# Kernel optimization log

Hardware: AMD Instinct MI355X
Metric: run time of the kernel (lower is better)

Reference implementation:

```python
import jax, jax.numpy as jnp
import numpy as np

EMBED_DIM = 768
HIDDEN_DIM = 384          # max(embed_dim // 2, 128)
NUM_HEADS = 12
HEAD_DIM = EMBED_DIM // NUM_HEADS
LAYER_VOCAB = 4           # len(target_layers)
THRESHOLD = 0.5
MIN_KEEP_RATIO = 0.1
B, N = 8, 1024


def setup_inputs() -> dict:
    key = jax.random.key(0)
    ks = jax.random.split(key, 12)
    std = 0.02
    return {
        "tokens": jax.random.normal(ks[0], (B, N, EMBED_DIM), jnp.float32),
        "layer_token_idx": 1,
        # actor params
        "layer_emb": jax.random.normal(ks[1], (LAYER_VOCAB, EMBED_DIM), jnp.float32) * std,
        "ln_g": jnp.ones((EMBED_DIM,), jnp.float32),
        "ln_b": jnp.zeros((EMBED_DIM,), jnp.float32),
        "w1": jax.random.normal(ks[2], (HIDDEN_DIM, EMBED_DIM), jnp.float32) * std,
        "b1": jnp.zeros((HIDDEN_DIM,), jnp.float32),
        "w2": jax.random.normal(ks[3], (HIDDEN_DIM, HIDDEN_DIM), jnp.float32) * std,
        "b2": jnp.zeros((HIDDEN_DIM,), jnp.float32),
        "w3": jax.random.normal(ks[4], (1, HIDDEN_DIM), jnp.float32) * std,
        "b3": jnp.zeros((1,), jnp.float32),
        # attention params (timm-style)
        "qkv_w": jax.random.normal(ks[5], (3 * EMBED_DIM, EMBED_DIM), jnp.float32) * std,
        "qkv_b": jnp.zeros((3 * EMBED_DIM,), jnp.float32),
        "proj_w": jax.random.normal(ks[6], (EMBED_DIM, EMBED_DIM), jnp.float32) * std,
        "proj_b": jnp.zeros((EMBED_DIM,), jnp.float32),
    }


def _layernorm(x, g, b, eps=1e-5):
    mu = x.mean(-1, keepdims=True)
    var = ((x - mu) ** 2).mean(-1, keepdims=True)
    return (x - mu) * jax.lax.rsqrt(var + eps) * g + b


def _forward(tokens, layer_token_idx, layer_emb, ln_g, ln_b, w1, b1, w2, b2, w3, b3,
             qkv_w, qkv_b, proj_w, proj_b):
    Bsz, Ntok, C = tokens.shape
    # --- MAPPOActor: logits ---
    ctx = tokens + layer_emb[layer_token_idx]               # broadcast [C]
    ctx = ctx + ctx.mean(axis=1, keepdims=True)             # global context
    h = _layernorm(ctx, ln_g, ln_b)
    h = jax.nn.gelu(h @ w1.T + b1, approximate=False)
    h = jax.nn.gelu(h @ w2.T + b2, approximate=False)
    logits = (h @ w3.T + b3).squeeze(-1)                    # [B, N]
    probs = jax.nn.sigmoid(logits)
    # --- compute_mask: threshold + min-keep topk correction ---
    binary = probs >= THRESHOLD                             # [B, N] bool
    min_keep = max(int(Ntok * MIN_KEEP_RATIO), 1)
    min_keep = min(min_keep, Ntok)
    _, topk_idx = jax.lax.top_k(probs, min_keep)            # [B, min_keep]
    fixed = jnp.zeros((Bsz, Ntok), bool).at[jnp.arange(Bsz)[:, None], topk_idx].set(True)
    need_fix = binary.sum(-1) < min_keep                    # [B]
    mask = jnp.where(need_fix[:, None], fixed, binary)
    mask = mask.at[:, 0].set(True)
    # --- masked attention (timm style) ---
    qkv = tokens @ qkv_w.T + qkv_b                          # [B, N, 3C]
    qkv = qkv.reshape(Bsz, Ntok, 3, NUM_HEADS, HEAD_DIM).transpose(2, 0, 3, 1, 4)
    q, k, v = qkv[0], qkv[1], qkv[2]                        # [B, H, N, D]
    q = q * (HEAD_DIM ** -0.5)
    scores = jnp.einsum("bhnd,bhmd->bhnm", q, k)            # [B, H, N, N]
    neg = jnp.finfo(scores.dtype).min
    scores = jnp.where(mask[:, None, None, :], scores, neg)
    attn = jax.nn.softmax(scores, axis=-1)
    v = v * mask[:, None, :, None].astype(v.dtype)
    out = jnp.einsum("bhnm,bhmd->bhnd", attn, v)
    out = out.transpose(0, 2, 1, 3).reshape(Bsz, Ntok, C)
    out = out @ proj_w.T + proj_b
    out = out * mask[..., None].astype(out.dtype)           # zero_out_queries=True
    return out


def reference(tokens, layer_token_idx, layer_emb, ln_g, ln_b, w1, b1, w2, b2, w3, b3,
              qkv_w, qkv_b, proj_w, proj_b):
    return _forward(tokens, layer_token_idx, layer_emb, ln_g, ln_b, w1, b1, w2, b2,
                    w3, b3, qkv_w, qkv_b, proj_w, proj_b)
```

## Files before the change

### kernel.cpp

```cpp
#include <hip/hip_runtime.h>
#include <cstdint>
#include <cmath>

#define EMBED 768
#define HID 384
#define NHEAD 12
#define HDIM 64
#define BATCH 8
#define NTOK 1024
#define MINKEEP 102

using f32x4  = __attribute__((ext_vector_type(4))) float;
using short8 = __attribute__((ext_vector_type(8))) short;
using short4v = __attribute__((ext_vector_type(4))) short;
using half8  = __attribute__((ext_vector_type(8))) _Float16;

__device__ inline short f2bf(float f) {
  unsigned u = __float_as_uint(f);
  u += 0x7fffu + ((u >> 16) & 1u);
  return (short)(u >> 16);
}
__device__ inline float bf2f(short s) {
  return __uint_as_float(((unsigned)(unsigned short)s) << 16);
}
__device__ inline unsigned pack_bf2(float lo, float hi) {
  unsigned ul = __float_as_uint(lo);
  ul += 0x7fffu + ((ul >> 16) & 1u);
  unsigned uh = __float_as_uint(hi);
  uh += 0x7fffu + ((uh >> 16) & 1u);
  return (ul >> 16) | (uh & 0xffff0000u);
}
__device__ inline void split2h(float v, short& h, short& m) {
  _Float16 h0 = (_Float16)v;
  float r = v - (float)h0;
  _Float16 m0 = (_Float16)r;
  h = __builtin_bit_cast(short, h0);
  m = __builtin_bit_cast(short, m0);
}

__global__ __launch_bounds__(256) void prep_kernel(
    const float* __restrict__ qkv_w, short* __restrict__ wq_bf,
    const float* __restrict__ proj_w, short* __restrict__ wp_bf,
    const float* __restrict__ w1, short* __restrict__ w1h, short* __restrict__ w1m,
    const float* __restrict__ w2, short* __restrict__ w2h, short* __restrict__ w2m,
    const float* __restrict__ layer_emb, const int* __restrict__ lidx,
    float* __restrict__ addvec) {
  int blk = blockIdx.x, tid = threadIdx.x;
  if (blk < 2304) {
    const float* in = (blk < 1728) ? qkv_w : proj_w;
    short* out = (blk < 1728) ? wq_bf : wp_bf;
    int i = (blk < 1728 ? blk : blk - 1728) * 256 + tid;
    float4 f = ((const float4*)in)[i];
    short4v s;
    s[0] = f2bf(f.x); s[1] = f2bf(f.y); s[2] = f2bf(f.z); s[3] = f2bf(f.w);
    ((short4v*)out)[i] = s;
  } else if (blk < 2736) {
    const float* in = (blk < 2592) ? w1 : w2;
    short* oh = (blk < 2592) ? w1h : w2h;
    short* om = (blk < 2592) ? w1m : w2m;
    int i = (blk < 2592 ? blk - 2304 : blk - 2592) * 256 + tid;
    float4 f = ((const float4*)in)[i];
    short4v h, m;
    short th, tm;
    split2h(f.x, th, tm); h[0] = th; m[0] = tm;
    split2h(f.y, th, tm); h[1] = th; m[1] = tm;
    split2h(f.z, th, tm); h[2] = th; m[2] = tm;
    split2h(f.w, th, tm); h[3] = th; m[3] = tm;
    ((short4v*)oh)[i] = h;
    ((short4v*)om)[i] = m;
  } else {
    int i = (blk - 2736) * 256 + tid;
    int c = i & (EMBED - 1);
    c = i % EMBED;
    addvec[i] = 2.0f * layer_emb[lidx[0] * EMBED + c];
  }
}

__global__ __launch_bounds__(768) void colmean_kernel(
    const float* __restrict__ tokens, float* __restrict__ addvec) {
  int b = blockIdx.x, chunk = blockIdx.y, c = threadIdx.x;
  const float* tb = tokens + ((size_t)b * NTOK + chunk * 64) * EMBED + c;
  float s = 0.f;
#pragma unroll 8
  for (int n = 0; n < 64; ++n) s += tb[(size_t)n * EMBED];
  atomicAdd(&addvec[b * EMBED + c], s * (1.0f / NTOK));
}

__global__ __launch_bounds__(256) void ln_split_kernel(
    const float* __restrict__ tokens, const float* __restrict__ addvec,
    const float* __restrict__ gamma, const float* __restrict__ beta,
    short* __restrict__ xh, short* __restrict__ xm,
    short* __restrict__ tok_bf) {
  int row = blockIdx.x;
  int b = row >> 10;
  __shared__ float s_row[EMBED];
  __shared__ float s_red[4];
  const float* tr = tokens + (size_t)row * EMBED;
  const float* av = addvec + b * EMBED;
  float lsum = 0.f;
  for (int c = threadIdx.x; c < EMBED; c += 256) {
    float t = tr[c];
    tok_bf[(size_t)row * EMBED + c] = f2bf(t);
    float v = t + av[c];
    s_row[c] = v;
    lsum += v;
  }
  for (int o = 32; o; o >>= 1) lsum += __shfl_down(lsum, o, 64);
  int wid = threadIdx.x >> 6;
  if ((threadIdx.x & 63) == 0) s_red[wid] = lsum;
  __syncthreads();
  float mu = (s_red[0] + s_red[1] + s_red[2] + s_red[3]) * (1.f / EMBED);
  float lss = 0.f;
  for (int c = threadIdx.x; c < EMBED; c += 256) {
    float d = s_row[c] - mu;
    lss += d * d;
  }
  for (int o = 32; o; o >>= 1) lss += __shfl_down(lss, o, 64);
  __syncthreads();
  if ((threadIdx.x & 63) == 0) s_red[wid] = lss;
  __syncthreads();
  float var = (s_red[0] + s_red[1] + s_red[2] + s_red[3]) * (1.f / EMBED);
  float rinv = 1.0f / sqrtf(var + 1e-5f);
  for (int c = threadIdx.x; c < EMBED; c += 256) {
    float v = (s_row[c] - mu) * rinv * gamma[c] + beta[c];
    short h, m;
    split2h(v, h, m);
    size_t idx = (size_t)row * EMBED + c;
    xh[idx] = h; xm[idx] = m;
  }
}

__device__ inline float gelu_exact(float x) {
  return 0.5f * x * (1.0f + erff(x * 0.70710678118654752f));
}

template <int OUT>
__global__ __launch_bounds__(256) void gemm_split_kernel(
    const short* __restrict__ Ah, const short* __restrict__ Am,
    const short* __restrict__ Wh, const short* __restrict__ Wm,
    const float* __restrict__ bias, short* __restrict__ Ch,
    short* __restrict__ Cm, const float* __restrict__ w3,
    float* __restrict__ lgt, int M, int N, int K) {
  __shared__ short sA[2][64][40];
  __shared__ short sW[2][64][40];
  int tid = threadIdx.x;
  int w = tid >> 6, l = tid & 63, lg = l >> 4, lb = l & 15;
  int wr = (w >> 1) * 32, wc = (w & 1) * 32;
  int row0 = blockIdx.x * 64, col0 = blockIdx.y * 64;
  int srow = tid >> 2;
  int skk = (tid & 3) * 8;
  f32x4 acc0[2][2] = {}, acc1[2][2] = {};
  short8 ra0, ra1, rw0, rw1;
  {
    size_t aoff = (size_t)(row0 + srow) * K + skk;
    size_t woff = (size_t)(col0 + srow) * K + skk;
    ra0 = *(const short8*)(Ah + aoff);
    ra1 = *(const short8*)(Am + aoff);
    rw0 = *(const short8*)(Wh + woff);
    rw1 = *(const short8*)(Wm + woff);
  }
  for (int k0 = 0; k0 < K; k0 += 32) {
    __syncthreads();
    *(short8*)&sA[0][srow][skk] = ra0;
    *(short8*)&sA[1][srow][skk] = ra1;
    *(short8*)&sW[0][srow][skk] = rw0;
    *(short8*)&sW[1][srow][skk] = rw1;
    __syncthreads();
    if (k0 + 32 < K) {
      size_t aoff = (size_t)(row0 + srow) * K + k0 + 32 + skk;
      size_t woff = (size_t)(col0 + srow) * K + k0 + 32 + skk;
      ra0 = *(const short8*)(Ah + aoff);
      ra1 = *(const short8*)(Am + aoff);
      rw0 = *(const short8*)(Wh + woff);
      rw1 = *(const short8*)(Wm + woff);
    }
    half8 ah[2], am[2], bh[2], bm[2];
#pragma unroll
    for (int i = 0; i < 2; ++i) {
      ah[i] = *(half8*)&sA[0][wr + i * 16 + lb][lg * 8];
      am[i] = *(half8*)&sA[1][wr + i * 16 + lb][lg * 8];
      bh[i] = *(half8*)&sW[0][wc + i * 16 + lb][lg * 8];
      bm[i] = *(half8*)&sW[1][wc + i * 16 + lb][lg * 8];
    }
#pragma unroll
    for (int i = 0; i < 2; ++i)
#pragma unroll
      for (int j = 0; j < 2; ++j) {
        f32x4 c0 = acc0[i][j];
        f32x4 c1 = acc1[i][j];
        c0 = __builtin_amdgcn_mfma_f32_16x16x32_f16(ah[i], bh[j], c0, 0, 0, 0);
        c1 = __builtin_amdgcn_mfma_f32_16x16x32_f16(ah[i], bm[j], c1, 0, 0, 0);
        c0 = __builtin_amdgcn_mfma_f32_16x16x32_f16(am[i], bh[j], c0, 0, 0, 0);
        acc0[i][j] = c0;
        acc1[i][j] = c1;
      }
  }
  if (OUT == 0) {
#pragma unroll
    for (int i = 0; i < 2; ++i) {
#pragma unroll
      for (int j = 0; j < 2; ++j) {
#pragma unroll
        for (int r = 0; r < 4; ++r) {
          int grow = row0 + wr + i * 16 + lg * 4 + r;
          int gcol = col0 + wc + j * 16 + lb;
          float g = gelu_exact(acc0[i][j][r] + acc1[i][j][r] + bias[gcol]);
          size_t idx = (size_t)grow * N + gcol;
          short h, m;
          split2h(g, h, m);
          Ch[idx] = h; Cm[idx] = m;
        }
      }
    }
  } else {
    float part[2][4];
#pragma unroll
    for (int i = 0; i < 2; ++i)
#pragma unroll
      for (int r = 0; r < 4; ++r) part[i][r] = 0.f;
#pragma unroll
    for (int i = 0; i < 2; ++i) {
#pragma unroll
      for (int j = 0; j < 2; ++j) {
#pragma unroll
        for (int r = 0; r < 4; ++r) {
          int gcol = col0 + wc + j * 16 + lb;
          float g = gelu_exact(acc0[i][j][r] + acc1[i][j][r] + bias[gcol]);
          part[i][r] += g * w3[gcol];
        }
      }
    }
#pragma unroll
    for (int i = 0; i < 2; ++i) {
#pragma unroll
      for (int r = 0; r < 4; ++r) {
        float v = part[i][r];
        v += __shfl_xor(v, 1);
        v += __shfl_xor(v, 2);
        v += __shfl_xor(v, 4);
        v += __shfl_xor(v, 8);
        if (lb == 0) atomicAdd(&lgt[row0 + wr + i * 16 + lg * 4 + r], v);
      }
    }
  }
}

__global__ __launch_bounds__(1024) void mask_kernel(
    const float* __restrict__ lgt, const float* __restrict__ b3,
    int* __restrict__ kidx, int* __restrict__ kc, float* __restrict__ biasc) {
  int b = blockIdx.x, tid = threadIdx.x;
  __shared__ unsigned long long keys[1024];
  __shared__ int flag[1024];
  __shared__ int wsum[16];
  float v = lgt[b * NTOK + tid] + b3[0];
  bool bin = (v >= 0.0f);
  int wid = tid >> 6, lane = tid & 63;
  unsigned long long bal = __ballot(bin);
  if (lane == 0) wsum[wid] = __popcll(bal);
  __syncthreads();
  int total = 0;
  for (int q = 0; q < 16; ++q) total += wsum[q];
  int mv;
  if (total >= MINKEEP) {
    mv = bin ? 1 : 0;
  } else {
    flag[tid] = 0;
    unsigned u = __float_as_uint(v);
    u = (u & 0x80000000u) ? ~u : (u | 0x80000000u);
    keys[tid] = ((unsigned long long)u << 32) | (unsigned)(1023 - tid);
    __syncthreads();
    for (int k2 = 2; k2 <= 1024; k2 <<= 1) {
      for (int j = k2 >> 1; j > 0; j >>= 1) {
        int ixj = tid ^ j;
        if (ixj > tid) {
          unsigned long long a = keys[tid], c = keys[ixj];
          bool desc = ((tid & k2) == 0);
          if (desc ? (a < c) : (a > c)) {
            keys[tid] = c;
            keys[ixj] = a;
          }
        }
        __syncthreads();
      }
    }
    if (tid < MINKEEP) {
      int idx = 1023 - (int)(keys[tid] & 0xFFFFFFFFu);
      flag[idx] = 1;
    }
    __syncthreads();
    mv = flag[tid];
  }
  if (tid == 0) mv = 1;
  __syncthreads();
  unsigned long long fb = __ballot(mv != 0);
  if (lane == 0) wsum[wid] = __popcll(fb);
  __syncthreads();
  int base = 0, tot = 0;
  for (int q = 0; q < 16; ++q) {
    int vq = wsum[q];
    if (q < wid) base += vq;
    tot += vq;
  }
  int pre = base + __popcll(fb & ((1ull << lane) - 1ull));
  if (mv) {
    kidx[b * NTOK + pre] = tid;
    biasc[b * NTOK + pre] = 0.f;
  }
  if (tid >= tot) {
    kidx[b * NTOK + tid] = 0;
    biasc[b * NTOK + tid] = -3.0e38f;
  }
  if (tid == 0) kc[b] = tot;
}

__global__ __launch_bounds__(256) void qkv_gather_kernel(
    const short* __restrict__ tok_bf, const short* __restrict__ W,
    const float* __restrict__ bias, const int* __restrict__ kidx,
    const int* __restrict__ kc, short* __restrict__ qq,
    short* __restrict__ kk_, short* __restrict__ vv) {
  __shared__ short sA[128][72];
  __shared__ short sW[128][72];
  __shared__ int s_idx[128];
  int bx = blockIdx.x;
  int b = bx & 7, bt = bx >> 3;
  int kcb = kc[b];
  if (bt * 128 >= kcb) return;
  int tid = threadIdx.x;
  if (tid < 128) s_idx[tid] = kidx[b * NTOK + bt * 128 + tid];
  int w = tid >> 6, l = tid & 63, lg = l >> 4, lb = l & 15;
  int wr = (w >> 1) * 64, wc = (w & 1) * 64;
  int col0 = blockIdx.y * 128;
  int r_ = tid >> 3, kq = (tid & 7) * 8;
  __syncthreads();
  const short* Ab = tok_bf + (size_t)b * NTOK * EMBED;
  f32x4 acc[4][4] = {};
  short8 pa[4], pw[4];
#pragma unroll
  for (int t = 0; t < 4; ++t) {
    pa[t] = *(const short8*)(Ab + (size_t)s_idx[t * 32 + r_] * EMBED + kq);
    pw[t] = *(const short8*)(W + (size_t)(col0 + t * 32 + r_) * EMBED + kq);
  }
  for (int k0 = 0; k0 < EMBED; k0 += 64) {
    __syncthreads();
#pragma unroll
    for (int t = 0; t < 4; ++t) {
      *(short8*)&sA[t * 32 + r_][kq] = pa[t];
      *(short8*)&sW[t * 32 + r_][kq] = pw[t];
    }
    __syncthreads();
    if (k0 + 64 < EMBED) {
#pragma unroll
      for (int t = 0; t < 4; ++t) {
        pa[t] = *(const short8*)(Ab + (size_t)s_idx[t * 32 + r_] * EMBED +
                                 k0 + 64 + kq);
        pw[t] = *(const short8*)(W + (size_t)(col0 + t * 32 + r_) * EMBED +
                                 k0 + 64 + kq);
      }
    }
#pragma unroll
    for (int half = 0; half < 2; ++half) {
      short8 af[4], bfr[4];
#pragma unroll
      for (int i = 0; i < 4; ++i)
        af[i] = *(short8*)&sA[wr + i * 16 + lb][half * 32 + lg * 8];
#pragma unroll
      for (int j = 0; j < 4; ++j)
        bfr[j] = *(short8*)&sW[wc + j * 16 + lb][half * 32 + lg * 8];
#pragma unroll
      for (int i = 0; i < 4; ++i)
#pragma unroll
        for (int j = 0; j < 4; ++j)
          acc[i][j] = __builtin_amdgcn_mfma_f32_16x16x32_bf16(af[i], bfr[j],
                                                              acc[i][j], 0, 0, 0);
    }
  }
#pragma unroll
  for (int i = 0; i < 4; ++i) {
#pragma unroll
    for (int j = 0; j < 4; ++j) {
#pragma unroll
      for (int r = 0; r < 4; ++r) {
        int jrow = bt * 128 + wr + i * 16 + lg * 4 + r;
        int gcol = col0 + wc + j * 16 + lb;
        float val = acc[i][j][r] + bias[gcol];
        int which = gcol / EMBED;
        int rem = gcol - which * EMBED;
        int h = rem >> 6, d = rem & 63;
        size_t dst = ((size_t)(b * NHEAD + h) * NTOK + jrow) * HDIM + d;
        if (which == 0)
          qq[dst] = f2bf(val * 0.125f);
        else if (which == 1)
          kk_[dst] = f2bf(val);
        else
          vv[dst] = f2bf(val);
      }
    }
  }
}

__global__ __launch_bounds__(256) void vtrans_kernel(
    const short* __restrict__ Vb, short* __restrict__ VT) {
  int bh = blockIdx.y;
  int n0 = blockIdx.x * 64;
  __shared__ short st[64][72];
  int tid = threadIdx.x;
#pragma unroll
  for (int t = 0; t < 2; ++t) {
    int c = tid + t * 256;
    int n = c >> 3, ds = c & 7;
    *(short8*)&st[n][ds * 8] =
        *(const short8*)(Vb + ((size_t)bh * NTOK + n0 + n) * HDIM + ds * 8);
  }
  __syncthreads();
#pragma unroll
  for (int t = 0; t < 2; ++t) {
    int c = tid + t * 256;
    int d = c >> 3, ns = c & 7;
    short8 tmp;
#pragma unroll
    for (int jj = 0; jj < 8; ++jj) tmp[jj] = st[ns * 8 + jj][d];
    *(short8*)(VT + ((size_t)bh * HDIM + d) * NTOK + n0 + ns * 8) = tmp;
  }
}

#define ATTN_SWZ(row, colbyte) (((row)*128) + ((colbyte) ^ (((row)&7) << 4)))

__global__ __launch_bounds__(256) void attn_mfma3_kernel(
    const short* __restrict__ Qc, const short* __restrict__ Kc,
    const short* __restrict__ VTc, const float* __restrict__ biasc,
    const int* __restrict__ kc, short* __restrict__ ao) {
  __shared__ __align__(16) short sK[64 * 64];
  __shared__ __align__(16) short sVT[64 * 64];
  int bid = blockIdx.x;
  int xcd = bid & 7, slot = bid >> 3;
  int bh = xcd * 12 + (slot >> 3);
  int qt = slot & 7;
  int b = bh / NHEAD;
  int kcb = kc[b];
  if (qt * 128 >= kcb) return;
  int nt = (kcb + 63) >> 6;
  int tid = threadIdx.x;
  int w = tid >> 6, l = tid & 63, lg = l >> 4, lb = l & 15;
  int n0 = qt * 128 + w * 32;
  const short* Qp = Qc + ((size_t)bh * NTOK + n0) * HDIM;
  const short* Kp = Kc + (size_t)bh * NTOK * HDIM;
  const short* Vp = VTc + (size_t)bh * HDIM * NTOK;
  const float* bp = biasc + b * NTOK;

  short8 qf[2][2];
#pragma unroll
  for (int i = 0; i < 2; ++i)
#pragma unroll
    for (int hh = 0; hh < 2; ++hh)
      qf[i][hh] = *(const short8*)(Qp + (i * 16 + lb) * HDIM + hh * 32 + lg * 8);

  f32x4 acc[2][4] = {};
  float lr[2] = {0.f, 0.f};

  int srow = tid >> 3;
  int scol = (tid & 7) * 8;
  int scolb = scol * 2;
  short8 rk0, rk1, rv0, rv1;

#define ATTN_LOADT(m0_)                                                        \
  {                                                                            \
    rk0 = *(const short8*)(Kp + (size_t)((m0_) + srow) * HDIM + scol);         \
    rk1 = *(const short8*)(Kp + (size_t)((m0_) + srow + 32) * HDIM + scol);    \
    rv0 = *(const short8*)(Vp + (size_t)srow * NTOK + (m0_) + scol);           \
    rv1 = *(const short8*)(Vp + (size_t)(srow + 32) * NTOK + (m0_) + scol);    \
  }

  ATTN_LOADT(0);
  for (int t = 0; t < nt; ++t) {
    int m0 = t * 64;
    *(short8*)((char*)sK + ATTN_SWZ(srow, scolb)) = rk0;
    *(short8*)((char*)sK + ATTN_SWZ(srow + 32, scolb)) = rk1;
    *(short8*)((char*)sVT + ATTN_SWZ(srow, scolb)) = rv0;
    *(short8*)((char*)sVT + ATTN_SWZ(srow + 32, scolb)) = rv1;
    __syncthreads();
    if (t + 1 < nt) ATTN_LOADT(m0 + 64);

    f32x4 bias4[4];
#pragma unroll
    for (int s = 0; s < 4; ++s)
      bias4[s] = *(const f32x4*)(bp + m0 + s * 16 + lg * 4);

    f32x4 S[2][4];
#pragma unroll
    for (int s = 0; s < 4; ++s) {
      short8 kf0 = *(const short8*)((const char*)sK +
                                    ATTN_SWZ(s * 16 + lb, lg * 16));
      short8 kf1 = *(const short8*)((const char*)sK +
                                    ATTN_SWZ(s * 16 + lb, 64 + lg * 16));
#pragma unroll
      for (int i = 0; i < 2; ++i) {
        f32x4 c = bias4[s];
        c = __builtin_amdgcn_mfma_f32_16x16x32_bf16(kf0, qf[i][0], c, 0, 0, 0);
        c = __builtin_amdgcn_mfma_f32_16x16x32_bf16(kf1, qf[i][1], c, 0, 0, 0);
        S[i][s] = c;
      }
    }

    unsigned pk[2][4][2];
#pragma unroll
    for (int i = 0; i < 2; ++i) {
      float rs = 0.f;
#pragma unroll
      for (int s = 0; s < 4; ++s) {
        float p0 = __expf(S[i][s][0]);
        float p1 = __expf(S[i][s][1]);
        float p2 = __expf(S[i][s][2]);
        float p3 = __expf(S[i][s][3]);
        rs += (p0 + p1) + (p2 + p3);
        pk[i][s][0] = pack_bf2(p0, p1);
        pk[i][s][1] = pack_bf2(p2, p3);
      }
      rs += __shfl_xor(rs, 16);
      rs += __shfl_xor(rs, 32);
      lr[i] += rs;
    }

    bool hi = (lg & 2) != 0;
    int srcl = ((lg & 1) * 2) * 16 + lb;
#pragma unroll
    for (int t2 = 0; t2 < 2; ++t2) {
      short8 vf[4];
#pragma unroll
      for (int u = 0; u < 4; ++u)
        vf[u] = *(const short8*)((const char*)sVT +
                                 ATTN_SWZ(u * 16 + lb, t2 * 64 + lg * 16));
#pragma unroll
      for (int i = 0; i < 2; ++i) {
        int a0 = __shfl((int)pk[i][2 * t2][0], srcl);
        int b0 = __shfl((int)pk[i][2 * t2 + 1][0], srcl);
        int a1 = __shfl((int)pk[i][2 * t2][1], srcl);
        int b1 = __shfl((int)pk[i][2 * t2 + 1][1], srcl);
        int a2 = __shfl((int)pk[i][2 * t2][0], srcl + 16);
        int b2 = __shfl((int)pk[i][2 * t2 + 1][0], srcl + 16);
        int a3 = __shfl((int)pk[i][2 * t2][1], srcl + 16);
        int b3 = __shfl((int)pk[i][2 * t2 + 1][1], srcl + 16);
        union { short8 s8; int u[4]; } pa;
        pa.u[0] = hi ? b0 : a0;
        pa.u[1] = hi ? b1 : a1;
        pa.u[2] = hi ? b2 : a2;
        pa.u[3] = hi ? b3 : a3;
#pragma unroll
        for (int u = 0; u < 4; ++u)
          acc[i][u] = __builtin_amdgcn_mfma_f32_16x16x32_bf16(pa.s8, vf[u],
                                                              acc[i][u], 0, 0, 0);
      }
    }
    __syncthreads();
  }

  int h = bh - b * NHEAD;
#pragma unroll
  for (int i = 0; i < 2; ++i) {
#pragma unroll
    for (int r = 0; r < 4; ++r) {
      float inv = 1.0f / __shfl(lr[i], lg * 4 + r);
      int j = n0 + i * 16 + lg * 4 + r;
#pragma unroll
      for (int u = 0; u < 4; ++u) {
        ao[((size_t)b * NTOK + j) * EMBED + h * HDIM + u * 16 + lb] =
            f2bf(acc[i][u][r] * inv);
      }
    }
  }
}

__global__ __launch_bounds__(256) void proj_gather_kernel(
    const short* __restrict__ A, const short* __restrict__ W,
    const float* __restrict__ bias, const int* __restrict__ kidx,
    const int* __restrict__ kc, float* __restrict__ out) {
  __shared__ short sA[128][72];
  __shared__ short sW[128][72];
  __shared__ int s_idx[128];
  int bx = blockIdx.x;
  int b = bx & 7, bt = bx >> 3;
  int kcb = kc[b];
  if (bt * 128 >= kcb) return;
  int tid = threadIdx.x;
  if (tid < 128) s_idx[tid] = kidx[b * NTOK + bt * 128 + tid];
  int w = tid >> 6, l = tid & 63, lg = l >> 4, lb = l & 15;
  int wr = (w >> 1) * 64, wc = (w & 1) * 64;
  int col0 = blockIdx.y * 128;
  int r_ = tid >> 3, kq = (tid & 7) * 8;
  const short* Ab = A + ((size_t)b * NTOK + bt * 128) * EMBED;
  f32x4 acc[4][4] = {};
  short8 pa[4], pw[4];
#pragma unroll
  for (int t = 0; t < 4; ++t) {
    pa[t] = *(const short8*)(Ab + (size_t)(t * 32 + r_) * EMBED + kq);
    pw[t] = *(const short8*)(W + (size_t)(col0 + t * 32 + r_) * EMBED + kq);
  }
  for (int k0 = 0; k0 < EMBED; k0 += 64) {
    __syncthreads();
#pragma unroll
    for (int t = 0; t < 4; ++t) {
      *(short8*)&sA[t * 32 + r_][kq] = pa[t];
      *(short8*)&sW[t * 32 + r_][kq] = pw[t];
    }
    __syncthreads();
    if (k0 + 64 < EMBED) {
#pragma unroll
      for (int t = 0; t < 4; ++t) {
        pa[t] = *(const short8*)(Ab + (size_t)(t * 32 + r_) * EMBED + k0 + 64 + kq);
        pw[t] = *(const short8*)(W + (size_t)(col0 + t * 32 + r_) * EMBED + k0 + 64 + kq);
      }
    }
#pragma unroll
    for (int half = 0; half < 2; ++half) {
      short8 af[4], bfr[4];
#pragma unroll
      for (int i = 0; i < 4; ++i)
        af[i] = *(short8*)&sA[wr + i * 16 + lb][half * 32 + lg * 8];
#pragma unroll
      for (int j = 0; j < 4; ++j)
        bfr[j] = *(short8*)&sW[wc + j * 16 + lb][half * 32 + lg * 8];
#pragma unroll
      for (int i = 0; i < 4; ++i)
#pragma unroll
        for (int j = 0; j < 4; ++j)
          acc[i][j] = __builtin_amdgcn_mfma_f32_16x16x32_bf16(af[i], bfr[j],
                                                              acc[i][j], 0, 0, 0);
    }
  }
#pragma unroll
  for (int i = 0; i < 4; ++i) {
#pragma unroll
    for (int j = 0; j < 4; ++j) {
#pragma unroll
      for (int r = 0; r < 4; ++r) {
        int jloc = wr + i * 16 + lg * 4 + r;
        int jrow = bt * 128 + jloc;
        int gcol = col0 + wc + j * 16 + lb;
        if (jrow < kcb) {
          int n = s_idx[jloc];
          out[((size_t)b * NTOK + n) * EMBED + gcol] = acc[i][j][r] + bias[gcol];
        }
      }
    }
  }
}

extern "C" void kernel_launch(void* const* d_in, const int* in_sizes, int n_in,
                              void* d_out, int out_size, void* d_ws, size_t ws_size,
                              hipStream_t stream) {
  const float* tokens   = (const float*)d_in[0];
  const int*   lidx     = (const int*)d_in[1];
  const float* layer_emb= (const float*)d_in[2];
  const float* ln_g     = (const float*)d_in[3];
  const float* ln_b     = (const float*)d_in[4];
  const float* w1       = (const float*)d_in[5];
  const float* b1       = (const float*)d_in[6];
  const float* w2       = (const float*)d_in[7];
  const float* b2       = (const float*)d_in[8];
  const float* w3       = (const float*)d_in[9];
  const float* b3       = (const float*)d_in[10];
  const float* qkv_w    = (const float*)d_in[11];
  const float* qkv_b    = (const float*)d_in[12];
  const float* proj_w   = (const float*)d_in[13];
  const float* proj_b   = (const float*)d_in[14];
  float* out = (float*)d_out;
  float* ws = (float*)d_ws;

  float* addvec = ws;
  float* lgt    = ws + 6144;
  int*   kidx   = (int*)(ws + 14336);
  float* biasc  = ws + 22528;
  int*   kc     = (int*)(ws + 30720);
  short* tok_bf = (short*)(ws + 30736);
  short* wq_bf  = (short*)(ws + 3176464);
  short* wp_bf  = (short*)(ws + 4061200);
  short* w1h = (short*)(ws + 4356112);
  short* w1m = (short*)(ws + 4503568);
  short* w2h = (short*)(ws + 4798480);
  short* w2m = (short*)(ws + 4872208);
  const size_t X0 = 5019664;
  short* xh  = (short*)(ws + X0);
  short* xm  = (short*)(ws + X0 + 3145728);
  short* h1h = (short*)(ws + X0 + 9437184);
  short* h1m = (short*)(ws + X0 + 11010048);
  short* Qc   = (short*)(ws + X0);
  short* Kc   = (short*)(ws + X0 + 3145728);
  short* Vc   = (short*)(ws + X0 + 6291456);
  short* VTc  = (short*)(ws + X0 + 9437184);
  short* aoc  = (short*)(ws + X0 + 12582912);

  hipMemsetAsync(d_out, 0, (size_t)out_size * sizeof(float), stream);
  hipMemsetAsync(lgt, 0, BATCH * NTOK * sizeof(float), stream);

  prep_kernel<<<dim3(2760), dim3(256), 0, stream>>>(
      qkv_w, wq_bf, proj_w, wp_bf, w1, w1h, w1m, w2, w2h, w2m,
      layer_emb, lidx, addvec);

  colmean_kernel<<<dim3(BATCH, 16), dim3(768), 0, stream>>>(tokens, addvec);
  ln_split_kernel<<<dim3(BATCH * NTOK), dim3(256), 0, stream>>>(
      tokens, addvec, ln_g, ln_b, xh, xm, tok_bf);
  gemm_split_kernel<0><<<dim3(128, 6), dim3(256), 0, stream>>>(
      xh, xm, w1h, w1m, b1, h1h, h1m, nullptr, nullptr,
      BATCH * NTOK, HID, EMBED);
  gemm_split_kernel<1><<<dim3(128, 6), dim3(256), 0, stream>>>(
      h1h, h1m, w2h, w2m, b2, nullptr, nullptr, w3, lgt,
      BATCH * NTOK, HID, HID);
  mask_kernel<<<dim3(BATCH), dim3(1024), 0, stream>>>(lgt, b3, kidx, kc, biasc);

  qkv_gather_kernel<<<dim3(64, 18), dim3(256), 0, stream>>>(
      tok_bf, wq_bf, qkv_b, kidx, kc, Qc, Kc, Vc);
  vtrans_kernel<<<dim3(16, BATCH * NHEAD), dim3(256), 0, stream>>>(Vc, VTc);
  attn_mfma3_kernel<<<dim3(768), dim3(256), 0, stream>>>(
      Qc, Kc, VTc, biasc, kc, aoc);
  proj_gather_kernel<<<dim3(64, 6), dim3(256), 0, stream>>>(
      aoc, wp_bf, proj_b, kidx, kc, out);
}
```

Baseline: 166.4 us.

## Fuse V transpose into QKV epilogue and fold colmean into prep kernel

```diff
diff --git a/kernel.cpp b/kernel.cpp
--- a/kernel.cpp
+++ b/kernel.cpp
@@ -43,8 +43,8 @@
     const float* __restrict__ proj_w, short* __restrict__ wp_bf,
     const float* __restrict__ w1, short* __restrict__ w1h, short* __restrict__ w1m,
     const float* __restrict__ w2, short* __restrict__ w2h, short* __restrict__ w2m,
-    const float* __restrict__ layer_emb, const int* __restrict__ lidx,
-    float* __restrict__ addvec) {
+    const float* __restrict__ tokens, float* __restrict__ colsum,
+    float* __restrict__ lgt) {
   int blk = blockIdx.x, tid = threadIdx.x;
   if (blk < 2304) {
     const float* in = (blk < 1728) ? qkv_w : proj_w;
@@ -68,26 +68,28 @@
     split2h(f.w, th, tm); h[3] = th; m[3] = tm;
     ((short4v*)oh)[i] = h;
     ((short4v*)om)[i] = m;
+  } else if (blk < 2744) {
+    int i = (blk - 2736) * 256 + tid;
+    ((float4*)lgt)[i] = make_float4(0.f, 0.f, 0.f, 0.f);
   } else {
-    int i = (blk - 2736) * 256 + tid;
-    int c = i & (EMBED - 1);
-    c = i % EMBED;
-    addvec[i] = 2.0f * layer_emb[lidx[0] * EMBED + c];
-  }
-}
-
-__global__ __launch_bounds__(768) void colmean_kernel(
-    const float* __restrict__ tokens, float* __restrict__ addvec) {
-  int b = blockIdx.x, chunk = blockIdx.y, c = threadIdx.x;
-  const float* tb = tokens + ((size_t)b * NTOK + chunk * 64) * EMBED + c;
-  float s = 0.f;
+    int idx = blk - 2744;
+    int b = idx >> 4, chunk = idx & 15;
+    const float* tb = tokens + ((size_t)b * NTOK + chunk * 64) * EMBED;
+    float s0 = 0.f, s1 = 0.f, s2 = 0.f;
 #pragma unroll 8
-  for (int n = 0; n < 64; ++n) s += tb[(size_t)n * EMBED];
-  atomicAdd(&addvec[b * EMBED + c], s * (1.0f / NTOK));
+    for (int n = 0; n < 64; ++n) {
+      const float* r = tb + (size_t)n * EMBED;
+      s0 += r[tid]; s1 += r[tid + 256]; s2 += r[tid + 512];
+    }
+    atomicAdd(&colsum[b * EMBED + tid], s0);
+    atomicAdd(&colsum[b * EMBED + tid + 256], s1);
+    atomicAdd(&colsum[b * EMBED + tid + 512], s2);
+  }
 }
 
 __global__ __launch_bounds__(256) void ln_split_kernel(
-    const float* __restrict__ tokens, const float* __restrict__ addvec,
+    const float* __restrict__ tokens, const float* __restrict__ colsum,
+    const float* __restrict__ layer_emb, const int* __restrict__ lidx,
     const float* __restrict__ gamma, const float* __restrict__ beta,
     short* __restrict__ xh, short* __restrict__ xm,
     short* __restrict__ tok_bf) {
@@ -96,12 +98,13 @@
   __shared__ float s_row[EMBED];
   __shared__ float s_red[4];
   const float* tr = tokens + (size_t)row * EMBED;
-  const float* av = addvec + b * EMBED;
+  const float* cs = colsum + b * EMBED;
+  const float* eb = layer_emb + lidx[0] * EMBED;
   float lsum = 0.f;
   for (int c = threadIdx.x; c < EMBED; c += 256) {
     float t = tr[c];
     tok_bf[(size_t)row * EMBED + c] = f2bf(t);
-    float v = t + av[c];
+    float v = t + 2.0f * eb[c] + cs[c] * (1.0f / NTOK);
     s_row[c] = v;
     lsum += v;
   }
@@ -317,9 +320,10 @@
     const short* __restrict__ tok_bf, const short* __restrict__ W,
     const float* __restrict__ bias, const int* __restrict__ kidx,
     const int* __restrict__ kc, short* __restrict__ qq,
-    short* __restrict__ kk_, short* __restrict__ vv) {
-  __shared__ short sA[128][72];
-  __shared__ short sW[128][72];
+    short* __restrict__ kk_, short* __restrict__ VTc) {
+  __shared__ short smem[2 * 128 * 72];
+  short (*sA)[72] = (short(*)[72])smem;
+  short (*sW)[72] = (short(*)[72])(smem + 128 * 72);
   __shared__ int s_idx[128];
   int bx = blockIdx.x;
   int b = bx & 7, bt = bx >> 3;
@@ -374,6 +378,36 @@
                                                               acc[i][j], 0, 0, 0);
     }
   }
+  if (col0 >= 2 * EMBED) {
+    __syncthreads();
+    short (*sT)[136] = (short(*)[136])smem;
+#pragma unroll
+    for (int i = 0; i < 4; ++i) {
+#pragma unroll
+      for (int j = 0; j < 4; ++j) {
+        int col_local = wc + j * 16 + lb;
+        int jr0 = wr + i * 16 + lg * 4;
+        short4v v4;
+#pragma unroll
+        for (int r = 0; r < 4; ++r)
+          v4[r] = f2bf(acc[i][j][r] + bias[col0 + col_local]);
+        *(short4v*)&sT[col_local][jr0] = v4;
+      }
+    }
+    __syncthreads();
+    int rem = col0 - 2 * EMBED;
+#pragma unroll
+    for (int t = 0; t < 8; ++t) {
+      int c = tid + t * 256;
+      int rowl = c >> 4;
+      int off = (c & 15) * 8;
+      int vcol = rem + rowl;
+      int h = vcol >> 6, d = vcol & 63;
+      size_t dst = ((size_t)(b * NHEAD + h) * HDIM + d) * NTOK + bt * 128 + off;
+      *(short8*)(VTc + dst) = *(short8*)&sT[rowl][off];
+    }
+    return;
+  }
 #pragma unroll
   for (int i = 0; i < 4; ++i) {
 #pragma unroll
@@ -384,42 +418,15 @@
         int gcol = col0 + wc + j * 16 + lb;
         float val = acc[i][j][r] + bias[gcol];
         int which = gcol / EMBED;
-        int rem = gcol - which * EMBED;
-        int h = rem >> 6, d = rem & 63;
+        int rem2 = gcol - which * EMBED;
+        int h = rem2 >> 6, d = rem2 & 63;
         size_t dst = ((size_t)(b * NHEAD + h) * NTOK + jrow) * HDIM + d;
         if (which == 0)
           qq[dst] = f2bf(val * 0.125f);
-        else if (which == 1)
+        else
           kk_[dst] = f2bf(val);
-        else
-          vv[dst] = f2bf(val);
-      }
-    }
-  }
-}
-
-__global__ __launch_bounds__(256) void vtrans_kernel(
-    const short* __restrict__ Vb, short* __restrict__ VT) {
-  int bh = blockIdx.y;
-  int n0 = blockIdx.x * 64;
-  __shared__ short st[64][72];
-  int tid = threadIdx.x;
-#pragma unroll
-  for (int t = 0; t < 2; ++t) {
-    int c = tid + t * 256;
-    int n = c >> 3, ds = c & 7;
-    *(short8*)&st[n][ds * 8] =
-        *(const short8*)(Vb + ((size_t)bh * NTOK + n0 + n) * HDIM + ds * 8);
-  }
-  __syncthreads();
-#pragma unroll
-  for (int t = 0; t < 2; ++t) {
-    int c = tid + t * 256;
-    int d = c >> 3, ns = c & 7;
-    short8 tmp;
-#pragma unroll
-    for (int jj = 0; jj < 8; ++jj) tmp[jj] = st[ns * 8 + jj][d];
-    *(short8*)(VT + ((size_t)bh * HDIM + d) * NTOK + n0 + ns * 8) = tmp;
+      }
+    }
   }
 }
 
@@ -665,7 +672,7 @@
   float* out = (float*)d_out;
   float* ws = (float*)d_ws;
 
-  float* addvec = ws;
+  float* colsum = ws;
   float* lgt    = ws + 6144;
   int*   kidx   = (int*)(ws + 14336);
   float* biasc  = ws + 22528;
@@ -684,20 +691,18 @@
   short* h1m = (short*)(ws + X0 + 11010048);
   short* Qc   = (short*)(ws + X0);
   short* Kc   = (short*)(ws + X0 + 3145728);
-  short* Vc   = (short*)(ws + X0 + 6291456);
   short* VTc  = (short*)(ws + X0 + 9437184);
   short* aoc  = (short*)(ws + X0 + 12582912);
 
   hipMemsetAsync(d_out, 0, (size_t)out_size * sizeof(float), stream);
-  hipMemsetAsync(lgt, 0, BATCH * NTOK * sizeof(float), stream);
-
-  prep_kernel<<<dim3(2760), dim3(256), 0, stream>>>(
+  hipMemsetAsync(colsum, 0, BATCH * EMBED * sizeof(float), stream);
+
+  prep_kernel<<<dim3(2872), dim3(256), 0, stream>>>(
       qkv_w, wq_bf, proj_w, wp_bf, w1, w1h, w1m, w2, w2h, w2m,
-      layer_emb, lidx, addvec);
-
-  colmean_kernel<<<dim3(BATCH, 16), dim3(768), 0, stream>>>(tokens, addvec);
+      tokens, colsum, lgt);
+
   ln_split_kernel<<<dim3(BATCH * NTOK), dim3(256), 0, stream>>>(
-      tokens, addvec, ln_g, ln_b, xh, xm, tok_bf);
+      tokens, colsum, layer_emb, lidx, ln_g, ln_b, xh, xm, tok_bf);
   gemm_split_kernel<0><<<dim3(128, 6), dim3(256), 0, stream>>>(
       xh, xm, w1h, w1m, b1, h1h, h1m, nullptr, nullptr,
       BATCH * NTOK, HID, EMBED);
@@ -707,8 +712,7 @@
   mask_kernel<<<dim3(BATCH), dim3(1024), 0, stream>>>(lgt, b3, kidx, kc, biasc);
 
   qkv_gather_kernel<<<dim3(64, 18), dim3(256), 0, stream>>>(
-      tok_bf, wq_bf, qkv_b, kidx, kc, Qc, Kc, Vc);
-  vtrans_kernel<<<dim3(16, BATCH * NHEAD), dim3(256), 0, stream>>>(Vc, VTc);
+      tok_bf, wq_bf, qkv_b, kidx, kc, Qc, Kc, VTc);
   attn_mfma3_kernel<<<dim3(768), dim3(256), 0, stream>>>(
       Qc, Kc, VTc, biasc, kc, aoc);
   proj_gather_kernel<<<dim3(64, 6), dim3(256), 0, stream>>>(
```

New measurement: 155.9 us. -6.3%, faster.
